# Optimization experiments

Measured on AMD Instinct MI355X. Metric: run time of the kernel, lower is better.

Reference implementation:

```python
import jax, jax.numpy as jnp
import numpy as np

D_MODEL = 768
N_HEAD = 12
D_K = D_MODEL // N_HEAD  # 64, also d_v
B, S = 2, 2048


def setup_inputs() -> dict:
    key = jax.random.key(0)
    ks = jax.random.split(key, 8)
    scale = 1.0 / np.sqrt(D_MODEL)
    return {
        "q": jax.random.normal(ks[0], (B, S, D_MODEL), dtype=jnp.float32),
        "k": jax.random.normal(ks[1], (B, S, D_MODEL), dtype=jnp.float32),
        "v": jax.random.normal(ks[2], (B, S, D_MODEL), dtype=jnp.float32),
        "mask": jax.random.randint(ks[3], (B, 1, S, S), 0, 2, dtype=jnp.int32),
        # per-head projection weights, stacked over heads: [H, d_model, d_k]
        "Wq": jax.random.normal(ks[4], (N_HEAD, D_MODEL, D_K), dtype=jnp.float32) * scale,
        "Wk": jax.random.normal(ks[5], (N_HEAD, D_MODEL, D_K), dtype=jnp.float32) * scale,
        "Wv": jax.random.normal(ks[6], (N_HEAD, D_MODEL, D_K), dtype=jnp.float32) * scale,
        # output projection: [n_head*d_v, d_model]
        "Wo": jax.random.normal(ks[7], (N_HEAD * D_K, D_MODEL), dtype=jnp.float32) * scale,
    }


def reference(q, k, v, mask, Wq, Wk, Wv, Wo):
    # Per-head projections (batched over heads instead of a python loop)
    qh = jnp.einsum("bsd,hdk->bhsk", q, Wq)  # [B,H,S,d_k]
    kh = jnp.einsum("bsd,hdk->bhsk", k, Wk)
    vh = jnp.einsum("bsd,hdk->bhsk", v, Wv)
    # Scaled dot-product attention with full score matrix (faithful to source)
    scores = jnp.einsum("bhsk,bhtk->bhst", qh, kh) / jnp.sqrt(jnp.asarray(D_K, qh.dtype))
    scores = jnp.where(mask == 0, jnp.asarray(-1e9, scores.dtype), scores)
    attn = jax.nn.softmax(scores, axis=-1)  # [B,H,S,S]
    out = jnp.einsum("bhst,bhtk->bhsk", attn, vh)  # [B,H,S,d_k]
    # concat heads (matches torch.cat over head outputs along last dim)
    out = out.transpose(0, 2, 1, 3).reshape(out.shape[0], out.shape[2], -1)  # [B,S,H*d_k]
    return out @ Wo  # [B,S,d_model]
```

## Files before the change

### kernel.cpp

```cpp
#include <hip/hip_runtime.h>
#include <stdint.h>

#define S_LEN 2048
#define NH 12
#define DM 768
#define DK 64
#define NB 2
#define MROWS (NB * S_LEN)

typedef __attribute__((ext_vector_type(8))) short short8;
typedef __attribute__((ext_vector_type(4))) float f32x4;

__device__ __forceinline__ unsigned short bf16rne(float f) {
    union { float f; uint32_t u; } v; v.f = f;
    return (unsigned short)((v.u + 0x7FFFu + ((v.u >> 16) & 1u)) >> 16);
}

__global__ __launch_bounds__(256) void cvt_kernel(
        const float* __restrict__ q, const float* __restrict__ k, const float* __restrict__ v,
        unsigned short* __restrict__ qb, unsigned short* __restrict__ kb, unsigned short* __restrict__ vb) {
    const float* src = (blockIdx.y == 0) ? q : (blockIdx.y == 1) ? k : v;
    unsigned short* dst = (blockIdx.y == 0) ? qb : (blockIdx.y == 1) ? kb : vb;
    int i = (blockIdx.x * 256 + threadIdx.x) * 4;
    float4 x = *(const float4*)(src + i);
    uint32_t lo = (uint32_t)bf16rne(x.x) | ((uint32_t)bf16rne(x.y) << 16);
    uint32_t hi = (uint32_t)bf16rne(x.z) | ((uint32_t)bf16rne(x.w) << 16);
    uint2 o = make_uint2(lo, hi);
    *(uint2*)(dst + i) = o;
}

__global__ __launch_bounds__(256) void wtrans_kernel(
        const float* __restrict__ Wq, const float* __restrict__ Wk,
        const float* __restrict__ Wv, const float* __restrict__ Wo,
        unsigned short* __restrict__ WqT, unsigned short* __restrict__ WkT,
        unsigned short* __restrict__ WvT, unsigned short* __restrict__ WoT) {
    int which = blockIdx.y;
    const float* W = (which == 0) ? Wq : (which == 1) ? Wk : (which == 2) ? Wv : Wo;
    unsigned short* WT = (which == 0) ? WqT : (which == 1) ? WkT : (which == 2) ? WvT : WoT;
    int idx = blockIdx.x * 256 + threadIdx.x;
    int n = idx / DM, kd = idx % DM;
    float val;
    if (which < 3) { int h = n >> 6, kk = n & 63; val = W[(h * DM + kd) * DK + kk]; }
    else          { val = W[kd * DM + n]; }
    WT[idx] = bf16rne(val);
}

__global__ __launch_bounds__(256) void mask_pack(const int* __restrict__ mask, uint32_t* __restrict__ pm) {
    int tid = blockIdx.x * 256 + threadIdx.x;
    int m = mask[tid];
    unsigned long long bm = __ballot(m != 0);
    if ((threadIdx.x & 63) == 0) {
        *(unsigned long long*)(pm + (tid >> 5)) = bm;
    }
}

__device__ __forceinline__ void gemm_core(const unsigned short* __restrict__ A,
                                          const unsigned short* __restrict__ BT,
                                          unsigned short* As, unsigned short* Bs,
                                          f32x4 (&acc)[4][4]) {
    const int tid = threadIdx.x;
    const int lane = tid & 63, wid = tid >> 6;
    const int ww = wid & 1, wh = wid >> 1;
    const int quad = lane >> 4, l16 = lane & 15;
    const int lr = lane >> 2;
    const int lc = (lane & 3) * 8;
    typedef __attribute__((address_space(1))) const unsigned int* gp1;
    typedef __attribute__((address_space(3))) unsigned int* lp3;
    const unsigned short* Ag = A + (size_t)(wid * 32 + lr) * DM + lc;
    const unsigned short* Bg = BT + (size_t)(wid * 32 + lr) * DM + lc;
    unsigned short* Al = &As[wid * 32 * 32];
    unsigned short* Bl = &Bs[wid * 32 * 32];
    for (int kt = 0; kt < DM; kt += 32) {
        __syncthreads();
        __builtin_amdgcn_global_load_lds((gp1)(const void*)(Ag + kt),            (lp3)(void*)Al,             16, 0, 0);
        __builtin_amdgcn_global_load_lds((gp1)(const void*)(Ag + 16 * DM + kt),  (lp3)(void*)(Al + 16 * 32), 16, 0, 0);
        __builtin_amdgcn_global_load_lds((gp1)(const void*)(Bg + kt),            (lp3)(void*)Bl,             16, 0, 0);
        __builtin_amdgcn_global_load_lds((gp1)(const void*)(Bg + 16 * DM + kt),  (lp3)(void*)(Bl + 16 * 32), 16, 0, 0);
        __syncthreads();
        short8 af[4], bf[4];
#pragma unroll
        for (int i = 0; i < 4; ++i) af[i] = *(const short8*)&As[(wh * 64 + i * 16 + l16) * 32 + quad * 8];
#pragma unroll
        for (int j = 0; j < 4; ++j) bf[j] = *(const short8*)&Bs[(ww * 64 + j * 16 + l16) * 32 + quad * 8];
#pragma unroll
        for (int i = 0; i < 4; ++i)
#pragma unroll
            for (int j = 0; j < 4; ++j)
                acc[i][j] = __builtin_amdgcn_mfma_f32_16x16x32_bf16(af[i], bf[j], acc[i][j], 0, 0, 0);
    }
}

__global__ __launch_bounds__(256) void proj_gemm(
        const unsigned short* __restrict__ qb, const unsigned short* __restrict__ kb,
        const unsigned short* __restrict__ vb,
        const unsigned short* __restrict__ WqT, const unsigned short* __restrict__ WkT,
        const unsigned short* __restrict__ WvT,
        unsigned short* __restrict__ qh, unsigned short* __restrict__ kh,
        unsigned short* __restrict__ vhT) {
    __shared__ __align__(16) unsigned short As[128 * 32];
    __shared__ __align__(16) unsigned short Bs[128 * 32];
    const int z = blockIdx.z;
    const unsigned short* A = (z == 0) ? qb : (z == 1) ? kb : vb;
    const unsigned short* BT = (z == 0) ? WqT : (z == 1) ? WkT : WvT;
    f32x4 acc[4][4] = {};
    gemm_core(A + (size_t)blockIdx.x * 128 * DM, BT + (size_t)blockIdx.y * 128 * DM, As, Bs, acc);

    const int tid = threadIdx.x;
    const int lane = tid & 63, wid = tid >> 6;
    const int ww = wid & 1, wh = wid >> 1;
    const int quad = lane >> 4, l16 = lane & 15;
    const int row0 = blockIdx.x * 128 + wh * 64;
    const int col0 = blockIdx.y * 128 + ww * 64;
    if (z < 2) {
        unsigned short* C = z ? kh : qh;
#pragma unroll
        for (int i = 0; i < 4; ++i)
#pragma unroll
            for (int j = 0; j < 4; ++j)
#pragma unroll
                for (int r = 0; r < 4; ++r)
                    C[(size_t)(row0 + i * 16 + quad * 4 + r) * DM + col0 + j * 16 + l16] = bf16rne(acc[i][j][r]);
    } else {
#pragma unroll
        for (int i = 0; i < 4; ++i)
#pragma unroll
            for (int j = 0; j < 4; ++j) {
                int row = row0 + i * 16 + quad * 4;
                int col = col0 + j * 16 + l16;
                int bb = row >> 11, s = row & 2047;
                int hh = col >> 6, d = col & 63;
                uint32_t lo = (uint32_t)bf16rne(acc[i][j][0]) | ((uint32_t)bf16rne(acc[i][j][1]) << 16);
                uint32_t hi = (uint32_t)bf16rne(acc[i][j][2]) | ((uint32_t)bf16rne(acc[i][j][3]) << 16);
                uint2 o = make_uint2(lo, hi);
                *(uint2*)&vhT[(size_t)((bb * NH + hh) * DK + d) * S_LEN + s] = o;
            }
    }
}

__global__ __launch_bounds__(256) void attn_kernel(
        const unsigned short* __restrict__ qh, const unsigned short* __restrict__ kh,
        const unsigned short* __restrict__ vhT, const uint32_t* __restrict__ pm,
        unsigned short* __restrict__ pob, float* __restrict__ lsb) {
    const int qt = blockIdx.x, h = blockIdx.y;
    const int b = blockIdx.z >> 1, ks = blockIdx.z & 1;
    const int tid = threadIdx.x, w = tid >> 6, lane = tid & 63;
    const int quad = lane >> 4, l16 = lane & 15;
    __shared__ __align__(16) unsigned short Ks[64 * 72];
    __shared__ __align__(16) unsigned short Vs[64 * 72];
    __shared__ __align__(16) unsigned short Ps[4][32 * 72];

    const int qrow0 = qt * 128 + w * 32;
    short8 qf[2][2];
#pragma unroll
    for (int mi = 0; mi < 2; ++mi) {
        const size_t qbase = (size_t)(b * S_LEN + qrow0 + mi * 16 + l16) * DM + h * DK;
        qf[mi][0] = *(const short8*)&qh[qbase + quad * 8];
        qf[mi][1] = *(const short8*)&qh[qbase + 32 + quad * 8];
    }
    short8 of = {};
    if (l16 == 0) {
#pragma unroll
        for (int j = 0; j < 8; ++j) of[j] = (short)0x3F80;
    }

    f32x4 out[2][4] = {};
    f32x4 outl[2] = {};

    const int srow = tid >> 2, scol = (tid & 3) << 4;
    const unsigned short* Kg = kh + (size_t)b * S_LEN * DM + h * DK;
    const unsigned short* Vg = vhT + (size_t)((b * NH + h) * DK) * S_LEN;
    const uint32_t* pmb = pm + (size_t)(b * S_LEN + qrow0 + quad * 4) * 64;
    const float SCL = 0.18033688011112042f;
    const float FM = 12.0f;
    const int kt0 = ks * (S_LEN / 2);

    for (int kt = kt0; kt < kt0 + S_LEN / 2; kt += 64) {
        __syncthreads();
        *(short8*)&Ks[srow * 72 + scol]     = *(const short8*)&Kg[(size_t)(kt + srow) * DM + scol];
        *(short8*)&Ks[srow * 72 + scol + 8] = *(const short8*)&Kg[(size_t)(kt + srow) * DM + scol + 8];
        *(short8*)&Vs[srow * 72 + scol]     = *(const short8*)&Vg[(size_t)srow * S_LEN + kt + scol];
        *(short8*)&Vs[srow * 72 + scol + 8] = *(const short8*)&Vg[(size_t)srow * S_LEN + kt + scol + 8];
        __syncthreads();

        uint2 mw[2][4];
#pragma unroll
        for (int mi = 0; mi < 2; ++mi)
#pragma unroll
            for (int r = 0; r < 4; ++r)
                mw[mi][r] = *(const uint2*)&pmb[(size_t)(mi * 16 + r) * 64 + (kt >> 5)];

#pragma unroll
        for (int cb = 0; cb < 4; ++cb) {
            short8 kf0 = *(const short8*)&Ks[(cb * 16 + l16) * 72 + quad * 8];
            short8 kf1 = *(const short8*)&Ks[(cb * 16 + l16) * 72 + 32 + quad * 8];
            const int boff = ((cb & 1) << 4) + l16;
#pragma unroll
            for (int mi = 0; mi < 2; ++mi) {
                f32x4 zz = {0.f, 0.f, 0.f, 0.f};
                zz = __builtin_amdgcn_mfma_f32_16x16x32_bf16(qf[mi][0], kf0, zz, 0, 0, 0);
                zz = __builtin_amdgcn_mfma_f32_16x16x32_bf16(qf[mi][1], kf1, zz, 0, 0, 0);
#pragma unroll
                for (int r = 0; r < 4; ++r) {
                    float e = __builtin_amdgcn_exp2f(fmaf(zz[r], SCL, -FM));
                    uint32_t mword = (cb >> 1) ? mw[mi][r].y : mw[mi][r].x;
                    int32_t mneg = __builtin_amdgcn_sbfe((int32_t)mword, boff, 1);
                    uint32_t up = (__float_as_uint(e) & (uint32_t)mneg) + 0x8000u;
                    Ps[w][(mi * 16 + quad * 4 + r) * 72 + cb * 16 + l16] = (unsigned short)(up >> 16);
                }
            }
        }

        short8 pf0[2], pf1[2];
#pragma unroll
        for (int mi = 0; mi < 2; ++mi) {
            pf0[mi] = *(const short8*)&Ps[w][(mi * 16 + l16) * 72 + quad * 8];
            pf1[mi] = *(const short8*)&Ps[w][(mi * 16 + l16) * 72 + 32 + quad * 8];
        }
#pragma unroll
        for (int cb2 = 0; cb2 < 4; ++cb2) {
            short8 vf0 = *(const short8*)&Vs[(cb2 * 16 + l16) * 72 + quad * 8];
            short8 vf1 = *(const short8*)&Vs[(cb2 * 16 + l16) * 72 + 32 + quad * 8];
#pragma unroll
            for (int mi = 0; mi < 2; ++mi) {
                out[mi][cb2] = __builtin_amdgcn_mfma_f32_16x16x32_bf16(pf0[mi], vf0, out[mi][cb2], 0, 0, 0);
                out[mi][cb2] = __builtin_amdgcn_mfma_f32_16x16x32_bf16(pf1[mi], vf1, out[mi][cb2], 0, 0, 0);
            }
        }
#pragma unroll
        for (int mi = 0; mi < 2; ++mi) {
            outl[mi] = __builtin_amdgcn_mfma_f32_16x16x32_bf16(pf0[mi], of, outl[mi], 0, 0, 0);
            outl[mi] = __builtin_amdgcn_mfma_f32_16x16x32_bf16(pf1[mi], of, outl[mi], 0, 0, 0);
        }
    }

    const int pz = b * 2 + ks;
#pragma unroll
    for (int mi = 0; mi < 2; ++mi) {
#pragma unroll
        for (int r = 0; r < 4; ++r) {
            float l = outl[mi][r];
#pragma unroll
            for (int d = 1; d < 16; d <<= 1) l += __shfl_xor(l, d);
            const int row = qrow0 + mi * 16 + quad * 4 + r;
            if (l16 == 0)
                lsb[((size_t)pz * NH + h) * S_LEN + row] = l;
#pragma unroll
            for (int cb2 = 0; cb2 < 4; ++cb2)
                pob[((size_t)pz * S_LEN + row) * DM + h * DK + cb2 * 16 + l16] = bf16rne(out[mi][cb2][r]);
        }
    }
}

__global__ __launch_bounds__(256) void merge_kernel(const unsigned short* __restrict__ pob,
                                                    const float* __restrict__ lsb,
                                                    unsigned short* __restrict__ ao) {
    int t = blockIdx.x * 256 + threadIdx.x;
    int sg = t / 192;
    int c = (t - sg * 192) * 4;
    int b = sg >> 11, s = sg & 2047, h = c >> 6;
    float l = lsb[((size_t)(b * 2) * NH + h) * S_LEN + s] +
              lsb[((size_t)(b * 2 + 1) * NH + h) * S_LEN + s];
    float rl = 1.f / fmaxf(l, 1e-37f);
    uint2 a0 = *(const uint2*)&pob[((size_t)(b * 2) * S_LEN + s) * DM + c];
    uint2 a1 = *(const uint2*)&pob[((size_t)(b * 2 + 1) * S_LEN + s) * DM + c];
    float f0 = __uint_as_float((a0.x & 0xFFFFu) << 16) + __uint_as_float((a1.x & 0xFFFFu) << 16);
    float f1 = __uint_as_float((a0.x >> 16) << 16)     + __uint_as_float((a1.x >> 16) << 16);
    float f2 = __uint_as_float((a0.y & 0xFFFFu) << 16) + __uint_as_float((a1.y & 0xFFFFu) << 16);
    float f3 = __uint_as_float((a0.y >> 16) << 16)     + __uint_as_float((a1.y >> 16) << 16);
    uint32_t lo = (uint32_t)bf16rne(f0 * rl) | ((uint32_t)bf16rne(f1 * rl) << 16);
    uint32_t hi = (uint32_t)bf16rne(f2 * rl) | ((uint32_t)bf16rne(f3 * rl) << 16);
    uint2 o = make_uint2(lo, hi);
    *(uint2*)&ao[(size_t)sg * DM + c] = o;
}

__global__ __launch_bounds__(256) void out_gemm(const unsigned short* __restrict__ ao,
                                                const unsigned short* __restrict__ WoT,
                                                float* __restrict__ C) {
    __shared__ __align__(16) unsigned short As[128 * 32];
    __shared__ __align__(16) unsigned short Bs[128 * 32];
    f32x4 acc[4][4] = {};
    gemm_core(ao + (size_t)blockIdx.x * 128 * DM, WoT + (size_t)blockIdx.y * 128 * DM, As, Bs, acc);
    const int tid = threadIdx.x;
    const int lane = tid & 63, wid = tid >> 6;
    const int ww = wid & 1, wh = wid >> 1;
    const int quad = lane >> 4, l16 = lane & 15;
    const int row0 = blockIdx.x * 128 + wh * 64;
    const int col0 = blockIdx.y * 128 + ww * 64;
#pragma unroll
    for (int i = 0; i < 4; ++i)
#pragma unroll
        for (int j = 0; j < 4; ++j)
#pragma unroll
            for (int r = 0; r < 4; ++r)
                C[(size_t)(row0 + i * 16 + quad * 4 + r) * DM + col0 + j * 16 + l16] = acc[i][j][r];
}

extern "C" void kernel_launch(void* const* d_in, const int* in_sizes, int n_in,
                              void* d_out, int out_size, void* d_ws, size_t ws_size,
                              hipStream_t stream) {
    const float* q = (const float*)d_in[0];
    const float* k = (const float*)d_in[1];
    const float* v = (const float*)d_in[2];
    const int* mask = (const int*)d_in[3];
    const float* Wq = (const float*)d_in[4];
    const float* Wk = (const float*)d_in[5];
    const float* Wv = (const float*)d_in[6];
    const float* Wo = (const float*)d_in[7];
    float* out = (float*)d_out;

    char* ws = (char*)d_ws;
    size_t off = 0;
    auto alloc = [&](size_t bytes) {
        void* p = ws + off;
        off += (bytes + 255) & ~(size_t)255;
        return p;
    };
    const size_t MAT = (size_t)MROWS * DM * 2;
    const size_t WMAT = (size_t)DM * DM * 2;
    unsigned short* qb  = (unsigned short*)alloc(MAT);
    unsigned short* kb  = (unsigned short*)alloc(MAT);
    unsigned short* vb  = (unsigned short*)alloc(MAT);
    unsigned short* WqT = (unsigned short*)alloc(WMAT);
    unsigned short* WkT = (unsigned short*)alloc(WMAT);
    unsigned short* WvT = (unsigned short*)alloc(WMAT);
    unsigned short* WoT = (unsigned short*)alloc(WMAT);
    unsigned short* qh  = (unsigned short*)alloc(MAT);
    unsigned short* kh  = (unsigned short*)alloc(MAT);
    unsigned short* vhT = (unsigned short*)alloc(MAT);
    unsigned short* ao  = (unsigned short*)alloc(MAT);
    uint32_t* pmask     = (uint32_t*)alloc((size_t)NB * S_LEN * 64 * 4);

    unsigned short* pob = (unsigned short*)ws;
    float* lsb = (float*)(ws + (size_t)4 * S_LEN * DM * 2);

    cvt_kernel<<<dim3(3072, 3), 256, 0, stream>>>(q, k, v, qb, kb, vb);
    wtrans_kernel<<<dim3(2304, 4), 256, 0, stream>>>(Wq, Wk, Wv, Wo, WqT, WkT, WvT, WoT);
    mask_pack<<<dim3(32768), 256, 0, stream>>>(mask, pmask);
    proj_gemm<<<dim3(32, 6, 3), 256, 0, stream>>>(qb, kb, vb, WqT, WkT, WvT, qh, kh, vhT);
    attn_kernel<<<dim3(16, 12, 4), 256, 0, stream>>>(qh, kh, vhT, pmask, pob, lsb);
    merge_kernel<<<dim3(3072), 256, 0, stream>>>(pob, lsb, ao);
    out_gemm<<<dim3(32, 6), 256, 0, stream>>>(ao, WoT, out);
}
```

Before: 242.1 us.

## Shrink GEMM tiles to 64x128 and split-K the output projection with atomics

The projection and output GEMMs now use 64x128 tiles, doubling the block count so more of the GPU's compute units get work. The output GEMM also splits K in two and accumulates into the zeroed output with float atomics. This targets low occupancy from too few blocks (192 for out_gemm), at the cost of an extra memset, atomic traffic, lower per-block data reuse and nondeterministic summation order.

New measurement: 262.7 us. 8.5% more time.

```diff
diff --git a/kernel.cpp b/kernel.cpp
--- a/kernel.cpp
+++ b/kernel.cpp
@@ -54,36 +54,35 @@
     }
 }
 
-__device__ __forceinline__ void gemm_core(const unsigned short* __restrict__ A,
-                                          const unsigned short* __restrict__ BT,
-                                          unsigned short* As, unsigned short* Bs,
-                                          f32x4 (&acc)[4][4]) {
+__device__ __forceinline__ void gemm_core64(const unsigned short* __restrict__ A,
+                                            const unsigned short* __restrict__ BT,
+                                            unsigned short* As, unsigned short* Bs,
+                                            f32x4 (&acc)[2][4], int ktBegin, int ktEnd) {
     const int tid = threadIdx.x;
-    const int lane = tid & 63, wid = tid >> 6;
-    const int ww = wid & 1, wh = wid >> 1;
+    const int lane = tid & 63, w = tid >> 6;
+    const int mh = w & 1, nh = w >> 1;
     const int quad = lane >> 4, l16 = lane & 15;
     const int lr = lane >> 2;
     const int lc = (lane & 3) * 8;
     typedef __attribute__((address_space(1))) const unsigned int* gp1;
     typedef __attribute__((address_space(3))) unsigned int* lp3;
-    const unsigned short* Ag = A + (size_t)(wid * 32 + lr) * DM + lc;
-    const unsigned short* Bg = BT + (size_t)(wid * 32 + lr) * DM + lc;
-    unsigned short* Al = &As[wid * 32 * 32];
-    unsigned short* Bl = &Bs[wid * 32 * 32];
-    for (int kt = 0; kt < DM; kt += 32) {
+    const unsigned short* Ag = A + (size_t)(w * 16 + lr) * DM + lc;
+    const unsigned short* Bg = BT + (size_t)(w * 32 + lr) * DM + lc;
+    unsigned short* Al = &As[w * 16 * 32];
+    unsigned short* Bl = &Bs[w * 32 * 32];
+    for (int kt = ktBegin; kt < ktEnd; kt += 32) {
         __syncthreads();
-        __builtin_amdgcn_global_load_lds((gp1)(const void*)(Ag + kt),            (lp3)(void*)Al,             16, 0, 0);
-        __builtin_amdgcn_global_load_lds((gp1)(const void*)(Ag + 16 * DM + kt),  (lp3)(void*)(Al + 16 * 32), 16, 0, 0);
-        __builtin_amdgcn_global_load_lds((gp1)(const void*)(Bg + kt),            (lp3)(void*)Bl,             16, 0, 0);
-        __builtin_amdgcn_global_load_lds((gp1)(const void*)(Bg + 16 * DM + kt),  (lp3)(void*)(Bl + 16 * 32), 16, 0, 0);
+        __builtin_amdgcn_global_load_lds((gp1)(const void*)(Ag + kt),           (lp3)(void*)Al,             16, 0, 0);
+        __builtin_amdgcn_global_load_lds((gp1)(const void*)(Bg + kt),           (lp3)(void*)Bl,             16, 0, 0);
+        __builtin_amdgcn_global_load_lds((gp1)(const void*)(Bg + 16 * DM + kt), (lp3)(void*)(Bl + 16 * 32), 16, 0, 0);
         __syncthreads();
-        short8 af[4], bf[4];
-#pragma unroll
-        for (int i = 0; i < 4; ++i) af[i] = *(const short8*)&As[(wh * 64 + i * 16 + l16) * 32 + quad * 8];
-#pragma unroll
-        for (int j = 0; j < 4; ++j) bf[j] = *(const short8*)&Bs[(ww * 64 + j * 16 + l16) * 32 + quad * 8];
-#pragma unroll
-        for (int i = 0; i < 4; ++i)
+        short8 af[2], bf[4];
+#pragma unroll
+        for (int i = 0; i < 2; ++i) af[i] = *(const short8*)&As[(mh * 32 + i * 16 + l16) * 32 + quad * 8];
+#pragma unroll
+        for (int j = 0; j < 4; ++j) bf[j] = *(const short8*)&Bs[(nh * 64 + j * 16 + l16) * 32 + quad * 8];
+#pragma unroll
+        for (int i = 0; i < 2; ++i)
 #pragma unroll
             for (int j = 0; j < 4; ++j)
                 acc[i][j] = __builtin_amdgcn_mfma_f32_16x16x32_bf16(af[i], bf[j], acc[i][j], 0, 0, 0);
@@ -97,24 +96,24 @@
         const unsigned short* __restrict__ WvT,
         unsigned short* __restrict__ qh, unsigned short* __restrict__ kh,
         unsigned short* __restrict__ vhT) {
-    __shared__ __align__(16) unsigned short As[128 * 32];
+    __shared__ __align__(16) unsigned short As[64 * 32];
     __shared__ __align__(16) unsigned short Bs[128 * 32];
     const int z = blockIdx.z;
     const unsigned short* A = (z == 0) ? qb : (z == 1) ? kb : vb;
     const unsigned short* BT = (z == 0) ? WqT : (z == 1) ? WkT : WvT;
-    f32x4 acc[4][4] = {};
-    gemm_core(A + (size_t)blockIdx.x * 128 * DM, BT + (size_t)blockIdx.y * 128 * DM, As, Bs, acc);
+    f32x4 acc[2][4] = {};
+    gemm_core64(A + (size_t)blockIdx.x * 64 * DM, BT + (size_t)blockIdx.y * 128 * DM, As, Bs, acc, 0, DM);
 
     const int tid = threadIdx.x;
-    const int lane = tid & 63, wid = tid >> 6;
-    const int ww = wid & 1, wh = wid >> 1;
+    const int lane = tid & 63, w = tid >> 6;
+    const int mh = w & 1, nh = w >> 1;
     const int quad = lane >> 4, l16 = lane & 15;
-    const int row0 = blockIdx.x * 128 + wh * 64;
-    const int col0 = blockIdx.y * 128 + ww * 64;
+    const int row0 = blockIdx.x * 64 + mh * 32;
+    const int col0 = blockIdx.y * 128 + nh * 64;
     if (z < 2) {
         unsigned short* C = z ? kh : qh;
 #pragma unroll
-        for (int i = 0; i < 4; ++i)
+        for (int i = 0; i < 2; ++i)
 #pragma unroll
             for (int j = 0; j < 4; ++j)
 #pragma unroll
@@ -122,7 +121,7 @@
                     C[(size_t)(row0 + i * 16 + quad * 4 + r) * DM + col0 + j * 16 + l16] = bf16rne(acc[i][j][r]);
     } else {
 #pragma unroll
-        for (int i = 0; i < 4; ++i)
+        for (int i = 0; i < 2; ++i)
 #pragma unroll
             for (int j = 0; j < 4; ++j) {
                 int row = row0 + i * 16 + quad * 4;
@@ -276,23 +275,26 @@
 __global__ __launch_bounds__(256) void out_gemm(const unsigned short* __restrict__ ao,
                                                 const unsigned short* __restrict__ WoT,
                                                 float* __restrict__ C) {
-    __shared__ __align__(16) unsigned short As[128 * 32];
+    __shared__ __align__(16) unsigned short As[64 * 32];
     __shared__ __align__(16) unsigned short Bs[128 * 32];
-    f32x4 acc[4][4] = {};
-    gemm_core(ao + (size_t)blockIdx.x * 128 * DM, WoT + (size_t)blockIdx.y * 128 * DM, As, Bs, acc);
+    const int ks = blockIdx.z;
+    f32x4 acc[2][4] = {};
+    gemm_core64(ao + (size_t)blockIdx.x * 64 * DM, WoT + (size_t)blockIdx.y * 128 * DM,
+                As, Bs, acc, ks * (DM / 2), (ks + 1) * (DM / 2));
     const int tid = threadIdx.x;
-    const int lane = tid & 63, wid = tid >> 6;
-    const int ww = wid & 1, wh = wid >> 1;
+    const int lane = tid & 63, w = tid >> 6;
+    const int mh = w & 1, nh = w >> 1;
     const int quad = lane >> 4, l16 = lane & 15;
-    const int row0 = blockIdx.x * 128 + wh * 64;
-    const int col0 = blockIdx.y * 128 + ww * 64;
-#pragma unroll
-    for (int i = 0; i < 4; ++i)
+    const int row0 = blockIdx.x * 64 + mh * 32;
+    const int col0 = blockIdx.y * 128 + nh * 64;
+#pragma unroll
+    for (int i = 0; i < 2; ++i)
 #pragma unroll
         for (int j = 0; j < 4; ++j)
 #pragma unroll
             for (int r = 0; r < 4; ++r)
-                C[(size_t)(row0 + i * 16 + quad * 4 + r) * DM + col0 + j * 16 + l16] = acc[i][j][r];
+                unsafeAtomicAdd(&C[(size_t)(row0 + i * 16 + quad * 4 + r) * DM + col0 + j * 16 + l16],
+                                acc[i][j][r]);
 }
 
 extern "C" void kernel_launch(void* const* d_in, const int* in_sizes, int n_in,
@@ -333,11 +335,12 @@
     unsigned short* pob = (unsigned short*)ws;
     float* lsb = (float*)(ws + (size_t)4 * S_LEN * DM * 2);
 
+    hipMemsetAsync(d_out, 0, (size_t)out_size * sizeof(float), stream);
     cvt_kernel<<<dim3(3072, 3), 256, 0, stream>>>(q, k, v, qb, kb, vb);
     wtrans_kernel<<<dim3(2304, 4), 256, 0, stream>>>(Wq, Wk, Wv, Wo, WqT, WkT, WvT, WoT);
     mask_pack<<<dim3(32768), 256, 0, stream>>>(mask, pmask);
-    proj_gemm<<<dim3(32, 6, 3), 256, 0, stream>>>(qb, kb, vb, WqT, WkT, WvT, qh, kh, vhT);
+    proj_gemm<<<dim3(64, 6, 3), 256, 0, stream>>>(qb, kb, vb, WqT, WkT, WvT, qh, kh, vhT);
     attn_kernel<<<dim3(16, 12, 4), 256, 0, stream>>>(qh, kh, vhT, pmask, pob, lsb);
     merge_kernel<<<dim3(3072), 256, 0, stream>>>(pob, lsb, ao);
-    out_gemm<<<dim3(32, 6), 256, 0, stream>>>(ao, WoT, out);
-}
+    out_gemm<<<dim3(64, 6, 2), 256, 0, stream>>>(ao, WoT, out);
+}
```

## Fuse input conversion, merge, and weight prep into neighboring kernels

Applied to the files above, without the earlier changes.

Folds the fp32→bf16 conversion of q/k/v into the projection GEMM's A-tile load, and folds the split-K merge and normalization into the output GEMM's A-tile load. This removes the cvt and merge kernels along with their intermediate buffers. Mask packing and weight transposition now run in a single prep launch, and the transpose goes through an LDS tile so that global accesses are coalesced. The cost is that A tiles are now loaded through registers instead of direct-to-LDS loads, which adds conversion work and a padded LDS layout inside the GEMM main loop, and out_gemm repeats the merge reads for each of its 6 column blocks.

Result: no change. 246.5 us (+1.8%).

```diff
diff --git a/kernel.cpp b/kernel.cpp
--- a/kernel.cpp
+++ b/kernel.cpp
@@ -15,71 +15,104 @@
     union { float f; uint32_t u; } v; v.f = f;
     return (unsigned short)((v.u + 0x7FFFu + ((v.u >> 16) & 1u)) >> 16);
 }
-
-__global__ __launch_bounds__(256) void cvt_kernel(
-        const float* __restrict__ q, const float* __restrict__ k, const float* __restrict__ v,
-        unsigned short* __restrict__ qb, unsigned short* __restrict__ kb, unsigned short* __restrict__ vb) {
-    const float* src = (blockIdx.y == 0) ? q : (blockIdx.y == 1) ? k : v;
-    unsigned short* dst = (blockIdx.y == 0) ? qb : (blockIdx.y == 1) ? kb : vb;
-    int i = (blockIdx.x * 256 + threadIdx.x) * 4;
-    float4 x = *(const float4*)(src + i);
-    uint32_t lo = (uint32_t)bf16rne(x.x) | ((uint32_t)bf16rne(x.y) << 16);
-    uint32_t hi = (uint32_t)bf16rne(x.z) | ((uint32_t)bf16rne(x.w) << 16);
-    uint2 o = make_uint2(lo, hi);
-    *(uint2*)(dst + i) = o;
-}
-
-__global__ __launch_bounds__(256) void wtrans_kernel(
+__device__ __forceinline__ float bf2f(unsigned short u) {
+    return __uint_as_float(((uint32_t)u) << 16);
+}
+
+__global__ __launch_bounds__(256) void prep_kernel(
+        const int* __restrict__ mask, uint32_t* __restrict__ pm,
         const float* __restrict__ Wq, const float* __restrict__ Wk,
         const float* __restrict__ Wv, const float* __restrict__ Wo,
         unsigned short* __restrict__ WqT, unsigned short* __restrict__ WkT,
         unsigned short* __restrict__ WvT, unsigned short* __restrict__ WoT) {
-    int which = blockIdx.y;
+    const int bid = blockIdx.x, tid = threadIdx.x;
+    __shared__ unsigned short tile[64 * 65];
+    if (bid < 32768) {
+        int t = bid * 256 + tid;
+        int m = mask[t];
+        unsigned long long bm = __ballot(m != 0);
+        if ((tid & 63) == 0) *(unsigned long long*)(pm + (t >> 5)) = bm;
+        return;
+    }
+    const int bid2 = bid - 32768;
+    const int which = bid2 / 144;
+    const int tle = bid2 - which * 144;
+    const int tx = tle % 12, ty = tle / 12;
     const float* W = (which == 0) ? Wq : (which == 1) ? Wk : (which == 2) ? Wv : Wo;
     unsigned short* WT = (which == 0) ? WqT : (which == 1) ? WkT : (which == 2) ? WvT : WoT;
-    int idx = blockIdx.x * 256 + threadIdx.x;
-    int n = idx / DM, kd = idx % DM;
-    float val;
-    if (which < 3) { int h = n >> 6, kk = n & 63; val = W[(h * DM + kd) * DK + kk]; }
-    else          { val = W[kd * DM + n]; }
-    WT[idx] = bf16rne(val);
-}
-
-__global__ __launch_bounds__(256) void mask_pack(const int* __restrict__ mask, uint32_t* __restrict__ pm) {
-    int tid = blockIdx.x * 256 + threadIdx.x;
-    int m = mask[tid];
-    unsigned long long bm = __ballot(m != 0);
-    if ((threadIdx.x & 63) == 0) {
-        *(unsigned long long*)(pm + (tid >> 5)) = bm;
-    }
-}
-
-__device__ __forceinline__ void gemm_core(const unsigned short* __restrict__ A,
-                                          const unsigned short* __restrict__ BT,
-                                          unsigned short* As, unsigned short* Bs,
-                                          f32x4 (&acc)[4][4]) {
+    if (which < 3) {
+        int j = tid & 63, i0 = tid >> 6;
+#pragma unroll
+        for (int s = 0; s < 16; ++s) {
+            int i = i0 + s * 4;
+            tile[i * 65 + j] = bf16rne(W[((size_t)tx * DM + ty * 64 + i) * DK + j]);
+        }
+        __syncthreads();
+        int kd2 = tid & 63, k0 = tid >> 6;
+#pragma unroll
+        for (int s = 0; s < 16; ++s) {
+            int kk = k0 + s * 4;
+            WT[(size_t)(tx * 64 + kk) * DM + ty * 64 + kd2] = tile[kd2 * 65 + kk];
+        }
+    } else {
+        int j = tid & 63, i0 = tid >> 6;
+#pragma unroll
+        for (int s = 0; s < 16; ++s) {
+            int i = i0 + s * 4;
+            tile[i * 65 + j] = bf16rne(W[(size_t)(ty * 64 + i) * DM + tx * 64 + j]);
+        }
+        __syncthreads();
+        int ii = tid & 63, j0 = tid >> 6;
+#pragma unroll
+        for (int s = 0; s < 16; ++s) {
+            int jj = j0 + s * 4;
+            WT[(size_t)(tx * 64 + jj) * DM + ty * 64 + ii] = tile[ii * 65 + jj];
+        }
+    }
+}
+
+__global__ __launch_bounds__(256) void proj_gemm(
+        const float* __restrict__ q, const float* __restrict__ k, const float* __restrict__ v,
+        const unsigned short* __restrict__ WqT, const unsigned short* __restrict__ WkT,
+        const unsigned short* __restrict__ WvT,
+        unsigned short* __restrict__ qh, unsigned short* __restrict__ kh,
+        unsigned short* __restrict__ vhT) {
+    __shared__ __align__(16) unsigned short As[128 * 40];
+    __shared__ __align__(16) unsigned short Bs[128 * 32];
+    const int z = blockIdx.z;
+    const float* A = (z == 0) ? q : (z == 1) ? k : v;
+    const unsigned short* BT = (z == 0) ? WqT : (z == 1) ? WkT : WvT;
     const int tid = threadIdx.x;
     const int lane = tid & 63, wid = tid >> 6;
     const int ww = wid & 1, wh = wid >> 1;
     const int quad = lane >> 4, l16 = lane & 15;
-    const int lr = lane >> 2;
-    const int lc = (lane & 3) * 8;
+    const int arow = tid >> 1, ac0 = (tid & 1) * 16;
+    const float* Ag = A + (size_t)(blockIdx.x * 128 + arow) * DM + ac0;
+    const int lr = lane >> 2, lc = (lane & 3) * 8;
     typedef __attribute__((address_space(1))) const unsigned int* gp1;
     typedef __attribute__((address_space(3))) unsigned int* lp3;
-    const unsigned short* Ag = A + (size_t)(wid * 32 + lr) * DM + lc;
-    const unsigned short* Bg = BT + (size_t)(wid * 32 + lr) * DM + lc;
-    unsigned short* Al = &As[wid * 32 * 32];
+    const unsigned short* Bg = BT + (size_t)(blockIdx.y * 128 + wid * 32 + lr) * DM + lc;
     unsigned short* Bl = &Bs[wid * 32 * 32];
+    f32x4 acc[4][4] = {};
     for (int kt = 0; kt < DM; kt += 32) {
         __syncthreads();
-        __builtin_amdgcn_global_load_lds((gp1)(const void*)(Ag + kt),            (lp3)(void*)Al,             16, 0, 0);
-        __builtin_amdgcn_global_load_lds((gp1)(const void*)(Ag + 16 * DM + kt),  (lp3)(void*)(Al + 16 * 32), 16, 0, 0);
-        __builtin_amdgcn_global_load_lds((gp1)(const void*)(Bg + kt),            (lp3)(void*)Bl,             16, 0, 0);
-        __builtin_amdgcn_global_load_lds((gp1)(const void*)(Bg + 16 * DM + kt),  (lp3)(void*)(Bl + 16 * 32), 16, 0, 0);
+        __builtin_amdgcn_global_load_lds((gp1)(const void*)(Bg + kt),           (lp3)(void*)Bl,             16, 0, 0);
+        __builtin_amdgcn_global_load_lds((gp1)(const void*)(Bg + 16 * DM + kt), (lp3)(void*)(Bl + 16 * 32), 16, 0, 0);
+        float4 x0 = *(const float4*)(Ag + kt);
+        float4 x1 = *(const float4*)(Ag + kt + 4);
+        float4 x2 = *(const float4*)(Ag + kt + 8);
+        float4 x3 = *(const float4*)(Ag + kt + 12);
+        short8 h0, h1;
+        h0[0] = bf16rne(x0.x); h0[1] = bf16rne(x0.y); h0[2] = bf16rne(x0.z); h0[3] = bf16rne(x0.w);
+        h0[4] = bf16rne(x1.x); h0[5] = bf16rne(x1.y); h0[6] = bf16rne(x1.z); h0[7] = bf16rne(x1.w);
+        h1[0] = bf16rne(x2.x); h1[1] = bf16rne(x2.y); h1[2] = bf16rne(x2.z); h1[3] = bf16rne(x2.w);
+        h1[4] = bf16rne(x3.x); h1[5] = bf16rne(x3.y); h1[6] = bf16rne(x3.z); h1[7] = bf16rne(x3.w);
+        *(short8*)&As[arow * 40 + ac0] = h0;
+        *(short8*)&As[arow * 40 + ac0 + 8] = h1;
         __syncthreads();
         short8 af[4], bf[4];
 #pragma unroll
-        for (int i = 0; i < 4; ++i) af[i] = *(const short8*)&As[(wh * 64 + i * 16 + l16) * 32 + quad * 8];
+        for (int i = 0; i < 4; ++i) af[i] = *(const short8*)&As[(wh * 64 + i * 16 + l16) * 40 + quad * 8];
 #pragma unroll
         for (int j = 0; j < 4; ++j) bf[j] = *(const short8*)&Bs[(ww * 64 + j * 16 + l16) * 32 + quad * 8];
 #pragma unroll
@@ -88,27 +121,7 @@
             for (int j = 0; j < 4; ++j)
                 acc[i][j] = __builtin_amdgcn_mfma_f32_16x16x32_bf16(af[i], bf[j], acc[i][j], 0, 0, 0);
     }
-}
-
-__global__ __launch_bounds__(256) void proj_gemm(
-        const unsigned short* __restrict__ qb, const unsigned short* __restrict__ kb,
-        const unsigned short* __restrict__ vb,
-        const unsigned short* __restrict__ WqT, const unsigned short* __restrict__ WkT,
-        const unsigned short* __restrict__ WvT,
-        unsigned short* __restrict__ qh, unsigned short* __restrict__ kh,
-        unsigned short* __restrict__ vhT) {
-    __shared__ __align__(16) unsigned short As[128 * 32];
-    __shared__ __align__(16) unsigned short Bs[128 * 32];
-    const int z = blockIdx.z;
-    const unsigned short* A = (z == 0) ? qb : (z == 1) ? kb : vb;
-    const unsigned short* BT = (z == 0) ? WqT : (z == 1) ? WkT : WvT;
-    f32x4 acc[4][4] = {};
-    gemm_core(A + (size_t)blockIdx.x * 128 * DM, BT + (size_t)blockIdx.y * 128 * DM, As, Bs, acc);
-
-    const int tid = threadIdx.x;
-    const int lane = tid & 63, wid = tid >> 6;
-    const int ww = wid & 1, wh = wid >> 1;
-    const int quad = lane >> 4, l16 = lane & 15;
+
     const int row0 = blockIdx.x * 128 + wh * 64;
     const int col0 = blockIdx.y * 128 + ww * 64;
     if (z < 2) {
@@ -251,39 +264,59 @@
     }
 }
 
-__global__ __launch_bounds__(256) void merge_kernel(const unsigned short* __restrict__ pob,
-                                                    const float* __restrict__ lsb,
-                                                    unsigned short* __restrict__ ao) {
-    int t = blockIdx.x * 256 + threadIdx.x;
-    int sg = t / 192;
-    int c = (t - sg * 192) * 4;
-    int b = sg >> 11, s = sg & 2047, h = c >> 6;
-    float l = lsb[((size_t)(b * 2) * NH + h) * S_LEN + s] +
-              lsb[((size_t)(b * 2 + 1) * NH + h) * S_LEN + s];
-    float rl = 1.f / fmaxf(l, 1e-37f);
-    uint2 a0 = *(const uint2*)&pob[((size_t)(b * 2) * S_LEN + s) * DM + c];
-    uint2 a1 = *(const uint2*)&pob[((size_t)(b * 2 + 1) * S_LEN + s) * DM + c];
-    float f0 = __uint_as_float((a0.x & 0xFFFFu) << 16) + __uint_as_float((a1.x & 0xFFFFu) << 16);
-    float f1 = __uint_as_float((a0.x >> 16) << 16)     + __uint_as_float((a1.x >> 16) << 16);
-    float f2 = __uint_as_float((a0.y & 0xFFFFu) << 16) + __uint_as_float((a1.y & 0xFFFFu) << 16);
-    float f3 = __uint_as_float((a0.y >> 16) << 16)     + __uint_as_float((a1.y >> 16) << 16);
-    uint32_t lo = (uint32_t)bf16rne(f0 * rl) | ((uint32_t)bf16rne(f1 * rl) << 16);
-    uint32_t hi = (uint32_t)bf16rne(f2 * rl) | ((uint32_t)bf16rne(f3 * rl) << 16);
-    uint2 o = make_uint2(lo, hi);
-    *(uint2*)&ao[(size_t)sg * DM + c] = o;
-}
-
-__global__ __launch_bounds__(256) void out_gemm(const unsigned short* __restrict__ ao,
+__global__ __launch_bounds__(256) void out_gemm(const unsigned short* __restrict__ pob,
+                                                const float* __restrict__ lsb,
                                                 const unsigned short* __restrict__ WoT,
                                                 float* __restrict__ C) {
-    __shared__ __align__(16) unsigned short As[128 * 32];
+    __shared__ __align__(16) unsigned short As[128 * 40];
     __shared__ __align__(16) unsigned short Bs[128 * 32];
-    f32x4 acc[4][4] = {};
-    gemm_core(ao + (size_t)blockIdx.x * 128 * DM, WoT + (size_t)blockIdx.y * 128 * DM, As, Bs, acc);
     const int tid = threadIdx.x;
     const int lane = tid & 63, wid = tid >> 6;
     const int ww = wid & 1, wh = wid >> 1;
     const int quad = lane >> 4, l16 = lane & 15;
+    const int arow = tid >> 1, ac0 = (tid & 1) * 16;
+    const int m = blockIdx.x * 128 + arow;
+    const int bb = m >> 11, s = m & 2047;
+    const unsigned short* P0 = pob + ((size_t)(bb * 2) * S_LEN + s) * DM + ac0;
+    const unsigned short* P1 = pob + ((size_t)(bb * 2 + 1) * S_LEN + s) * DM + ac0;
+    const float* L0 = lsb + (size_t)(bb * 2) * NH * S_LEN + s;
+    const float* L1 = lsb + (size_t)(bb * 2 + 1) * NH * S_LEN + s;
+    const int lr = lane >> 2, lc = (lane & 3) * 8;
+    typedef __attribute__((address_space(1))) const unsigned int* gp1;
+    typedef __attribute__((address_space(3))) unsigned int* lp3;
+    const unsigned short* Bg = WoT + (size_t)(blockIdx.y * 128 + wid * 32 + lr) * DM + lc;
+    unsigned short* Bl = &Bs[wid * 32 * 32];
+    f32x4 acc[4][4] = {};
+    for (int kt = 0; kt < DM; kt += 32) {
+        __syncthreads();
+        __builtin_amdgcn_global_load_lds((gp1)(const void*)(Bg + kt),           (lp3)(void*)Bl,             16, 0, 0);
+        __builtin_amdgcn_global_load_lds((gp1)(const void*)(Bg + 16 * DM + kt), (lp3)(void*)(Bl + 16 * 32), 16, 0, 0);
+        const int h = (kt + ac0) >> 6;
+        float rl = 1.f / fmaxf(L0[(size_t)h * S_LEN] + L1[(size_t)h * S_LEN], 1e-37f);
+        short8 a0 = *(const short8*)(P0 + kt);
+        short8 a1 = *(const short8*)(P0 + kt + 8);
+        short8 c0 = *(const short8*)(P1 + kt);
+        short8 c1 = *(const short8*)(P1 + kt + 8);
+        short8 h0, h1;
+#pragma unroll
+        for (int i = 0; i < 8; ++i) {
+            h0[i] = bf16rne((bf2f((unsigned short)a0[i]) + bf2f((unsigned short)c0[i])) * rl);
+            h1[i] = bf16rne((bf2f((unsigned short)a1[i]) + bf2f((unsigned short)c1[i])) * rl);
+        }
+        *(short8*)&As[arow * 40 + ac0] = h0;
+        *(short8*)&As[arow * 40 + ac0 + 8] = h1;
+        __syncthreads();
+        short8 af[4], bf[4];
+#pragma unroll
+        for (int i = 0; i < 4; ++i) af[i] = *(const short8*)&As[(wh * 64 + i * 16 + l16) * 40 + quad * 8];
+#pragma unroll
+        for (int j = 0; j < 4; ++j) bf[j] = *(const short8*)&Bs[(ww * 64 + j * 16 + l16) * 32 + quad * 8];
+#pragma unroll
+        for (int i = 0; i < 4; ++i)
+#pragma unroll
+            for (int j = 0; j < 4; ++j)
+                acc[i][j] = __builtin_amdgcn_mfma_f32_16x16x32_bf16(af[i], bf[j], acc[i][j], 0, 0, 0);
+    }
     const int row0 = blockIdx.x * 128 + wh * 64;
     const int col0 = blockIdx.y * 128 + ww * 64;
 #pragma unroll
@@ -317,9 +350,6 @@
     };
     const size_t MAT = (size_t)MROWS * DM * 2;
     const size_t WMAT = (size_t)DM * DM * 2;
-    unsigned short* qb  = (unsigned short*)alloc(MAT);
-    unsigned short* kb  = (unsigned short*)alloc(MAT);
-    unsigned short* vb  = (unsigned short*)alloc(MAT);
     unsigned short* WqT = (unsigned short*)alloc(WMAT);
     unsigned short* WkT = (unsigned short*)alloc(WMAT);
     unsigned short* WvT = (unsigned short*)alloc(WMAT);
@@ -327,17 +357,12 @@
     unsigned short* qh  = (unsigned short*)alloc(MAT);
     unsigned short* kh  = (unsigned short*)alloc(MAT);
     unsigned short* vhT = (unsigned short*)alloc(MAT);
-    unsigned short* ao  = (unsigned short*)alloc(MAT);
     uint32_t* pmask     = (uint32_t*)alloc((size_t)NB * S_LEN * 64 * 4);
-
-    unsigned short* pob = (unsigned short*)ws;
-    float* lsb = (float*)(ws + (size_t)4 * S_LEN * DM * 2);
-
-    cvt_kernel<<<dim3(3072, 3), 256, 0, stream>>>(q, k, v, qb, kb, vb);
-    wtrans_kernel<<<dim3(2304, 4), 256, 0, stream>>>(Wq, Wk, Wv, Wo, WqT, WkT, WvT, WoT);
-    mask_pack<<<dim3(32768), 256, 0, stream>>>(mask, pmask);
-    proj_gemm<<<dim3(32, 6, 3), 256, 0, stream>>>(qb, kb, vb, WqT, WkT, WvT, qh, kh, vhT);
+    unsigned short* pob = (unsigned short*)alloc((size_t)4 * S_LEN * DM * 2);
+    float* lsb          = (float*)alloc((size_t)4 * NH * S_LEN * 4);
+
+    prep_kernel<<<dim3(32768 + 576), 256, 0, stream>>>(mask, pmask, Wq, Wk, Wv, Wo, WqT, WkT, WvT, WoT);
+    proj_gemm<<<dim3(32, 6, 3), 256, 0, stream>>>(q, k, v, WqT, WkT, WvT, qh, kh, vhT);
     attn_kernel<<<dim3(16, 12, 4), 256, 0, stream>>>(qh, kh, vhT, pmask, pob, lsb);
-    merge_kernel<<<dim3(3072), 256, 0, stream>>>(pob, lsb, ao);
-    out_gemm<<<dim3(32, 6), 256, 0, stream>>>(ao, WoT, out);
-}
+    out_gemm<<<dim3(32, 6), 256, 0, stream>>>(pob, lsb, WoT, out);
+}
```
